# Kernel tuning notes

Measured on AMD Instinct MI355X. Metric: run time of the kernel, lower is better.

The kernel has to match this reference:

```python
import jax, jax.numpy as jnp
import numpy as np

HIDDEN = 1024
N_HEADS = 16
HEAD_DIM = HIDDEN // N_HEADS
LN_EPS = 1e-5


def setup_inputs() -> dict:
    key = jax.random.key(0)
    ks = jax.random.split(key, 8)
    B, S = 4, 1024
    inp = {
        'input_tensor': jax.random.normal(ks[0], (B, S, HIDDEN), dtype=jnp.float32),
        'memory_tensor': jax.random.normal(ks[1], (B, S, HIDDEN), dtype=jnp.float32),
        'attention_mask': jnp.ones((B, S, S), dtype=jnp.float32),
        'wq': jax.random.normal(ks[2], (HIDDEN, HIDDEN), dtype=jnp.float32) * 0.02,
        'wk': jax.random.normal(ks[3], (HIDDEN, HIDDEN), dtype=jnp.float32) * 0.02,
        'wv': jax.random.normal(ks[4], (HIDDEN, HIDDEN), dtype=jnp.float32) * 0.02,
        'wo': jax.random.normal(ks[5], (HIDDEN, HIDDEN), dtype=jnp.float32) * 0.02,
        'ln_gamma': jnp.ones((HIDDEN,), dtype=jnp.float32),
        'ln_beta': jnp.zeros((HIDDEN,), dtype=jnp.float32),
        'seq_length': 1024,
        'enc_seq_length': 1024,
    }
    return inp


def _layernorm(x, gamma, beta):
    mu = jnp.mean(x, axis=-1, keepdims=True)
    var = jnp.mean(jnp.square(x - mu), axis=-1, keepdims=True)
    return (x - mu) * jax.lax.rsqrt(var + LN_EPS) * gamma + beta


def reference(input_tensor, memory_tensor, attention_mask, wq, wk, wv, wo,
              ln_gamma, ln_beta, seq_length, enc_seq_length):
    B = input_tensor.shape[0]
    S = seq_length
    x2d = input_tensor.reshape(-1, HIDDEN)            # [B*S, H]
    normed = _layernorm(x2d, ln_gamma, ln_beta)       # LayerPreprocess
    # is_encdec_att=False: memory = normed output (memory_tensor unused)
    mem = normed
    # torch nn.Linear(bias=False): y = x @ W.T
    q = (normed @ wq.T).reshape(B, S, N_HEADS, HEAD_DIM).transpose(0, 2, 1, 3)
    k = (mem @ wk.T).reshape(B, S, N_HEADS, HEAD_DIM).transpose(0, 2, 1, 3)
    v = (mem @ wv.T).reshape(B, S, N_HEADS, HEAD_DIM).transpose(0, 2, 1, 3)
    scale = 1.0 / np.sqrt(float(HEAD_DIM))
    scores = jnp.einsum('bhqd,bhkd->bhqk', q, k) * scale   # [B, H, S, S]
    scores = scores - 10000.0 * (1.0 - attention_mask[:, None, :, :])
    probs = jax.nn.softmax(scores, axis=-1)
    ctx = jnp.einsum('bhqk,bhkd->bhqd', probs, v)          # [B, H, S, dh]
    ctx = ctx.transpose(0, 2, 1, 3).reshape(B * S, HIDDEN)
    attn_out = ctx @ wo.T
    # LayerPostprocess (dropout=0): residual add with raw (pre-LN) input
    return attn_out + x2d
```

## Files before the change

### kernel.cpp

```cpp
#include <hip/hip_runtime.h>
#include <hip/hip_bf16.h>


typedef unsigned short u16;
typedef __attribute__((ext_vector_type(8))) short short8;
typedef __attribute__((ext_vector_type(4))) float f32x4;

__device__ __forceinline__ u16 f2bf(float f) {
  union { float f; unsigned u; } cv; cv.f = f;
  unsigned u = cv.u + 0x7fffu + ((cv.u >> 16) & 1u);
  return (u16)(u >> 16);
}

__device__ __forceinline__ float bf2f(u16 u) {
  union { unsigned u; float f; } cv; cv.u = ((unsigned)u) << 16;
  return cv.f;
}

__device__ __forceinline__ void gload_lds16(const void* g, void* l) {
  __builtin_amdgcn_global_load_lds(
      (const __attribute__((address_space(1))) void*)g,
      (__attribute__((address_space(3))) void*)l, 16, 0, 0);
}

__device__ __forceinline__ f32x4 mfma16(short8 a, short8 b, f32x4 c) {
  return __builtin_amdgcn_mfma_f32_16x16x32_bf16(a, b, c, 0, 0, 0);
}

__global__ __launch_bounds__(256) void ln_kernel(const float* __restrict__ x,
                                                 const float* __restrict__ gamma,
                                                 const float* __restrict__ beta,
                                                 u16* __restrict__ outn) {
  __shared__ float sm[4];
  const int row = blockIdx.x, t = threadIdx.x;
  float4 v = ((const float4*)(x + (size_t)row * 1024))[t];
  float s = v.x + v.y + v.z + v.w;
#pragma unroll
  for (int off = 32; off; off >>= 1) s += __shfl_down(s, off);
  if ((t & 63) == 0) sm[t >> 6] = s;
  __syncthreads();
  const float mu = (sm[0] + sm[1] + sm[2] + sm[3]) * (1.0f / 1024.0f);
  const float dx = v.x - mu, dy = v.y - mu, dz = v.z - mu, dw = v.w - mu;
  float vs = dx * dx + dy * dy + dz * dz + dw * dw;
  __syncthreads();
#pragma unroll
  for (int off = 32; off; off >>= 1) vs += __shfl_down(vs, off);
  if ((t & 63) == 0) sm[t >> 6] = vs;
  __syncthreads();
  const float var = (sm[0] + sm[1] + sm[2] + sm[3]) * (1.0f / 1024.0f);
  const float rstd = rsqrtf(var + 1e-5f);
  float4 g = ((const float4*)gamma)[t];
  float4 b = ((const float4*)beta)[t];
  uint2 pk;
  pk.x = (unsigned)f2bf(dx * rstd * g.x + b.x) | ((unsigned)f2bf(dy * rstd * g.y + b.y) << 16);
  pk.y = (unsigned)f2bf(dz * rstd * g.z + b.z) | ((unsigned)f2bf(dw * rstd * g.w + b.w) << 16);
  *(uint2*)&outn[(size_t)row * 1024 + t * 4] = pk;
}

__global__ __launch_bounds__(256) void cvt_w(const float* __restrict__ wq,
                                             const float* __restrict__ wk,
                                             const float* __restrict__ wv,
                                             const float* __restrict__ wo,
                                             u16* __restrict__ out) {
  const int i = blockIdx.x * 256 + threadIdx.x;
  const int e = i * 4;
  const int seg = e >> 20;
  const int off = e & 1048575;
  const float* src = (seg == 0) ? wq : (seg == 1) ? wk : (seg == 2) ? wv : wo;
  float4 v = *(const float4*)(src + off);
  uint2 pk;
  pk.x = (unsigned)f2bf(v.x) | ((unsigned)f2bf(v.y) << 16);
  pk.y = (unsigned)f2bf(v.z) | ((unsigned)f2bf(v.w) << 16);
  *(uint2*)&out[e] = pk;
}

__global__ __launch_bounds__(256) void cvt_bias(const float* __restrict__ mask,
                                                u16* __restrict__ bias) {
  const int tid = blockIdx.x * 256 + threadIdx.x;
  const int half = tid & 1;
  const int lg = (tid >> 1) & 3;
  const int kt = (tid >> 3) & 15;
  const int q  = (tid >> 7) & 1023;
  const int b  = tid >> 17;
  const float* src = mask + ((size_t)b * 1024 + q) * 1024 + kt * 64 + lg * 4;
  float4 v0 = *(const float4*)(src + (half * 2 + 0) * 16);
  float4 v1 = *(const float4*)(src + (half * 2 + 1) * 16);
  uint4 w;
  w.x = (unsigned)f2bf(fmaf(10000.f, v0.x, -10000.f)) |
        ((unsigned)f2bf(fmaf(10000.f, v0.y, -10000.f)) << 16);
  w.y = (unsigned)f2bf(fmaf(10000.f, v0.z, -10000.f)) |
        ((unsigned)f2bf(fmaf(10000.f, v0.w, -10000.f)) << 16);
  w.z = (unsigned)f2bf(fmaf(10000.f, v1.x, -10000.f)) |
        ((unsigned)f2bf(fmaf(10000.f, v1.y, -10000.f)) << 16);
  w.w = (unsigned)f2bf(fmaf(10000.f, v1.z, -10000.f)) |
        ((unsigned)f2bf(fmaf(10000.f, v1.w, -10000.f)) << 16);
  *(uint4*)&bias[(size_t)tid * 8] = w;
}

template <int MODE>
__global__ __launch_bounds__(256) void gemm_bt(const u16* __restrict__ A,
                                               const u16* __restrict__ Bm,
                                               u16* __restrict__ outQ, u16* __restrict__ outK,
                                               u16* __restrict__ outVt,
                                               float* __restrict__ outF,
                                               const float* __restrict__ resid) {
  constexpr int BK = 64, KK = 1024;
  __shared__ u16 As[128 * BK];
  __shared__ u16 Bs[128 * BK];
  const int m0 = blockIdx.y * 128, n0 = blockIdx.x * 128;
  const int t = threadIdx.x;
  const int wid = t >> 6, lane = t & 63;
  const int wm = (wid >> 1) * 64, wn = (wid & 1) * 64;
  const int lr = lane & 15, lg = lane >> 4;
  f32x4 acc[4][4] = {};
  const u16* aSrc = A + (size_t)(m0 + (t >> 3)) * KK + (t & 7) * 8;
  const u16* bSrc = Bm + (size_t)(n0 + (t >> 3)) * KK + (t & 7) * 8;

  for (int k0 = 0; k0 < KK; k0 += BK) {
    __syncthreads();
#pragma unroll
    for (int c = 0; c < 4; c++) {
      gload_lds16(aSrc + (size_t)c * 32 * KK + k0, As + c * 2048 + t * 8);
      gload_lds16(bSrc + (size_t)c * 32 * KK + k0, Bs + c * 2048 + t * 8);
    }
    __syncthreads();
    short8 af[4][2], bfr[4][2];
#pragma unroll
    for (int mi = 0; mi < 4; mi++)
#pragma unroll
      for (int kc = 0; kc < 2; kc++)
        af[mi][kc] = *(const short8*)&As[(wm + mi * 16 + lr) * BK + kc * 32 + lg * 8];
#pragma unroll
    for (int ni = 0; ni < 4; ni++)
#pragma unroll
      for (int kc = 0; kc < 2; kc++)
        bfr[ni][kc] = *(const short8*)&Bs[(wn + ni * 16 + lr) * BK + kc * 32 + lg * 8];
#pragma unroll
    for (int mi = 0; mi < 4; mi++)
#pragma unroll
      for (int ni = 0; ni < 4; ni++)
#pragma unroll
        for (int kc = 0; kc < 2; kc++)
          acc[mi][ni] = mfma16(af[mi][kc], bfr[ni][kc], acc[mi][ni]);
  }

#pragma unroll
  for (int mi = 0; mi < 4; mi++)
#pragma unroll
    for (int ni = 0; ni < 4; ni++)
#pragma unroll
      for (int r = 0; r < 4; r++) {
        const int i = m0 + wm + mi * 16 + lg * 4 + r;
        const int j = n0 + wn + ni * 16 + lr;
        const float val = acc[mi][ni][r];
        if (MODE == 0) {
          const int seg = j >> 10, jj = j & 1023;
          const int h = jj >> 6, d = jj & 63;
          const int b = i >> 10, s_ = i & 1023;
          if (seg == 0)      outQ[((size_t)(b * 16 + h) * 1024 + s_) * 64 + d] = f2bf(val * 0.125f);
          else if (seg == 1) outK[((size_t)(b * 16 + h) * 1024 + s_) * 64 + d] = f2bf(val);
          else               outVt[((size_t)(b * 16 + h) * 64 + d) * 1024 + s_] = f2bf(val);
        } else {
          const size_t o = (size_t)i * 1024 + j;
          outF[o] = val + resid[o];
        }
      }
}

__global__ __launch_bounds__(256) void flash_kernel(const u16* __restrict__ Qg,
                                                    const u16* __restrict__ Kg,
                                                    const u16* __restrict__ Vt,
                                                    const u16* __restrict__ bias,
                                                    u16* __restrict__ ctx) {
  const int h = blockIdx.x, qt = blockIdx.y, b = blockIdx.z;
  const int bh = b * 16 + h;
  __shared__ u16 Ks[2][4096];
  __shared__ u16 Vs[2][4096];
  __shared__ u16 Ps[4][1024];
  const int t = threadIdx.x, wid = t >> 6, lane = t & 63;
  const int lr = lane & 15, lg = lane >> 4;
  const int hR = lr & 7;
  const int qbase = qt * 64 + wid * 16;

  short8 qf0, qf1;
  {
    const u16* qrow = Qg + ((size_t)bh * 1024 + qbase + lr) * 64;
    qf0 = *(const short8*)(qrow + lg * 8);
    qf1 = *(const short8*)(qrow + 32 + lg * 8);
  }
  f32x4 octx[4] = {};
  float m_ln = -1e30f, l_ln = 0.0f;

  const u16* kS0 = Kg + (size_t)bh * 65536;
  const u16* vS0 = Vt + (size_t)bh * 65536;
  const int srow = t >> 3, scb = t & 7;

  const u16* bptr = bias + ((size_t)b * 1024 + qbase + lr) * 1024 + lg * 16;

  auto STAGE = [&](int nb, int kt) {
#pragma unroll
    for (int c = 0; c < 2; c++) {
      const int row = c * 32 + srow;
      const int sc = (scb ^ (row & 7)) * 8;
      gload_lds16(kS0 + (size_t)(kt * 64 + row) * 64 + sc, &Ks[nb][c * 2048 + t * 8]);
      gload_lds16(vS0 + (size_t)row * 1024 + kt * 64 + sc, &Vs[nb][c * 2048 + t * 8]);
    }
  };

  STAGE(0, 0);
  short8 bc0 = *(const short8*)(bptr);
  short8 bc1 = *(const short8*)(bptr + 8);
  asm volatile("s_waitcnt vmcnt(0)" ::: "memory");
  __builtin_amdgcn_s_barrier();
  __builtin_amdgcn_sched_barrier(0);

  int cur = 0;
  for (int kt = 0; kt < 16; kt++) {
    const int ktn = (kt < 15) ? kt + 1 : 15;
    STAGE(cur ^ 1, ktn);
    short8 bn0 = *(const short8*)(bptr + ktn * 64);
    short8 bn1 = *(const short8*)(bptr + ktn * 64 + 8);

    float sv[4][4];
#pragma unroll
    for (int kn = 0; kn < 4; kn++) {
      const int R = kn * 16 + lr;
      short8 kf0 = *(const short8*)&Ks[cur][R * 64 + ((lg ^ hR) << 3)];
      short8 kf1 = *(const short8*)&Ks[cur][R * 64 + (((lg + 4) ^ hR) << 3)];
      f32x4 s = {};
      s = mfma16(kf0, qf0, s);
      s = mfma16(kf1, qf1, s);
      short8 bsel = (kn < 2) ? bc0 : bc1;
#pragma unroll
      for (int r = 0; r < 4; r++)
        sv[kn][r] = s[r] + bf2f((u16)bsel[(kn & 1) * 4 + r]);
    }

    float mx0 = fmaxf(fmaxf(sv[0][0], sv[0][1]), fmaxf(sv[0][2], sv[0][3]));
    float mx1 = fmaxf(fmaxf(sv[1][0], sv[1][1]), fmaxf(sv[1][2], sv[1][3]));
    float mx2 = fmaxf(fmaxf(sv[2][0], sv[2][1]), fmaxf(sv[2][2], sv[2][3]));
    float mx3 = fmaxf(fmaxf(sv[3][0], sv[3][1]), fmaxf(sv[3][2], sv[3][3]));
    float mt = fmaxf(fmaxf(mx0, mx1), fmaxf(mx2, mx3));
    mt = fmaxf(mt, __shfl_xor(mt, 16));
    mt = fmaxf(mt, __shfl_xor(mt, 32));
    const float mn = fmaxf(m_ln, mt);
    const float f = __expf(m_ln - mn);
    m_ln = mn;
    float ps = 0.0f;
#pragma unroll
    for (int kn = 0; kn < 4; kn++) {
      float p0 = __expf(sv[kn][0] - mn), p1 = __expf(sv[kn][1] - mn);
      float p2 = __expf(sv[kn][2] - mn), p3 = __expf(sv[kn][3] - mn);
      sv[kn][0] = p0; sv[kn][1] = p1; sv[kn][2] = p2; sv[kn][3] = p3;
      ps += (p0 + p1) + (p2 + p3);
    }
    ps += __shfl_xor(ps, 16);
    ps += __shfl_xor(ps, 32);
    l_ln = l_ln * f + ps;

    float fb[4];
#pragma unroll
    for (int r = 0; r < 4; r++)
      fb[r] = __shfl(f, (lane & 48) | (lg * 4 + r), 64);
#pragma unroll
    for (int g = 0; g < 4; g++)
#pragma unroll
      for (int r = 0; r < 4; r++) octx[g][r] *= fb[r];

    const int swz = (lr & 7) << 1;
#pragma unroll
    for (int kn = 0; kn < 4; kn++) {
      uint2 w;
      w.x = (unsigned)f2bf(sv[kn][0]) | ((unsigned)f2bf(sv[kn][1]) << 16);
      w.y = (unsigned)f2bf(sv[kn][2]) | ((unsigned)f2bf(sv[kn][3]) << 16);
      *(uint2*)&Ps[wid][lr * 64 + (((kn * 4 + lg) ^ swz) << 2)] = w;
    }
    short8 pa0 = *(const short8*)&Ps[wid][lr * 64 + (((2 * lg) ^ swz) << 2)];
    short8 pa1 = *(const short8*)&Ps[wid][lr * 64 + (((8 + 2 * lg) ^ swz) << 2)];

#pragma unroll
    for (int g = 0; g < 4; g++) {
      const int R = g * 16 + lr;
      short8 vf0 = *(const short8*)&Vs[cur][R * 64 + ((lg ^ hR) << 3)];
      short8 vf1 = *(const short8*)&Vs[cur][R * 64 + (((lg + 4) ^ hR) << 3)];
      octx[g] = mfma16(pa0, vf0, octx[g]);
      octx[g] = mfma16(pa1, vf1, octx[g]);
    }

    asm volatile("s_waitcnt vmcnt(0)" ::: "memory");
    __builtin_amdgcn_s_barrier();
    __builtin_amdgcn_sched_barrier(0);
    cur ^= 1;
    bc0 = bn0; bc1 = bn1;
  }

  float lb[4];
#pragma unroll
  for (int r = 0; r < 4; r++)
    lb[r] = __shfl(l_ln, (lane & 48) | (lg * 4 + r), 64);
#pragma unroll
  for (int g = 0; g < 4; g++)
#pragma unroll
    for (int r = 0; r < 4; r++) {
      const int qr = qbase + lg * 4 + r;
      ctx[((size_t)b * 1024 + qr) * 1024 + h * 64 + g * 16 + lr] = f2bf(octx[g][r] / lb[r]);
    }
}

extern "C" void kernel_launch(void* const* d_in, const int* in_sizes, int n_in,
                              void* d_out, int out_size, void* d_ws, size_t ws_size,
                              hipStream_t stream) {
  const float* x     = (const float*)d_in[0];
  const float* mask  = (const float*)d_in[2];
  const float* wq    = (const float*)d_in[3];
  const float* wk    = (const float*)d_in[4];
  const float* wv    = (const float*)d_in[5];
  const float* wo    = (const float*)d_in[6];
  const float* gamma = (const float*)d_in[7];
  const float* beta  = (const float*)d_in[8];
  float* out = (float*)d_out;

  char* ws = (char*)d_ws;
  u16* normed = (u16*)(ws);
  u16* wcat   = (u16*)(ws + (8ull << 20));
  u16* Qg     = (u16*)(ws + (16ull << 20));
  u16* Kg     = (u16*)(ws + (24ull << 20));
  u16* Vtg    = (u16*)(ws + (32ull << 20));
  u16* ctx    = (u16*)(ws + (40ull << 20));
  u16* wo_bf  = wcat + 3072ull * 1024;
  u16* bias   = normed;

  ln_kernel<<<4096, 256, 0, stream>>>(x, gamma, beta, normed);
  cvt_w<<<4096, 256, 0, stream>>>(wq, wk, wv, wo, wcat);
  gemm_bt<0><<<dim3(24, 32), 256, 0, stream>>>(normed, wcat, Qg, Kg, Vtg, nullptr, nullptr);
  cvt_bias<<<2048, 256, 0, stream>>>(mask, bias);
  flash_kernel<<<dim3(16, 16, 4), 256, 0, stream>>>(Qg, Kg, Vtg, bias, ctx);
  gemm_bt<1><<<dim3(8, 32), 256, 0, stream>>>(ctx, wo_bf, nullptr, nullptr, nullptr, out, x);
}
```

Measured before the change: 254.4 us.

## Double-buffer GEMM, stage epilogue through LDS, read fp32 mask directly in flash

The GEMM now uses BK=32 double-buffered LDS staging with a swizzled layout, and s_setprio around the MFMA block. The QKV epilogue goes through LDS so Q/K/Vt are written with vectorised, coalesced stores instead of scattered 2-byte stores. The output GEMM uses 64-row tiles so it launches more blocks. The cvt_bias pass is removed and the flash kernel reads the fp32 mask directly, computing the additive bias in registers, at the cost of twice the mask bytes per tile and more registers.

```diff
diff --git a/kernel.cpp b/kernel.cpp
--- a/kernel.cpp
+++ b/kernel.cpp
@@ -10,11 +10,6 @@
   union { float f; unsigned u; } cv; cv.f = f;
   unsigned u = cv.u + 0x7fffu + ((cv.u >> 16) & 1u);
   return (u16)(u >> 16);
-}
-
-__device__ __forceinline__ float bf2f(u16 u) {
-  union { unsigned u; float f; } cv; cv.u = ((unsigned)u) << 16;
-  return cv.f;
 }
 
 __device__ __forceinline__ void gload_lds16(const void* g, void* l) {
@@ -74,29 +69,6 @@
   *(uint2*)&out[e] = pk;
 }
 
-__global__ __launch_bounds__(256) void cvt_bias(const float* __restrict__ mask,
-                                                u16* __restrict__ bias) {
-  const int tid = blockIdx.x * 256 + threadIdx.x;
-  const int half = tid & 1;
-  const int lg = (tid >> 1) & 3;
-  const int kt = (tid >> 3) & 15;
-  const int q  = (tid >> 7) & 1023;
-  const int b  = tid >> 17;
-  const float* src = mask + ((size_t)b * 1024 + q) * 1024 + kt * 64 + lg * 4;
-  float4 v0 = *(const float4*)(src + (half * 2 + 0) * 16);
-  float4 v1 = *(const float4*)(src + (half * 2 + 1) * 16);
-  uint4 w;
-  w.x = (unsigned)f2bf(fmaf(10000.f, v0.x, -10000.f)) |
-        ((unsigned)f2bf(fmaf(10000.f, v0.y, -10000.f)) << 16);
-  w.y = (unsigned)f2bf(fmaf(10000.f, v0.z, -10000.f)) |
-        ((unsigned)f2bf(fmaf(10000.f, v0.w, -10000.f)) << 16);
-  w.z = (unsigned)f2bf(fmaf(10000.f, v1.x, -10000.f)) |
-        ((unsigned)f2bf(fmaf(10000.f, v1.y, -10000.f)) << 16);
-  w.w = (unsigned)f2bf(fmaf(10000.f, v1.z, -10000.f)) |
-        ((unsigned)f2bf(fmaf(10000.f, v1.w, -10000.f)) << 16);
-  *(uint4*)&bias[(size_t)tid * 8] = w;
-}
-
 template <int MODE>
 __global__ __launch_bounds__(256) void gemm_bt(const u16* __restrict__ A,
                                                const u16* __restrict__ Bm,
@@ -104,73 +76,135 @@
                                                u16* __restrict__ outVt,
                                                float* __restrict__ outF,
                                                const float* __restrict__ resid) {
-  constexpr int BK = 64, KK = 1024;
-  __shared__ u16 As[128 * BK];
-  __shared__ u16 Bs[128 * BK];
-  const int m0 = blockIdx.y * 128, n0 = blockIdx.x * 128;
+  constexpr int BM = (MODE == 0) ? 128 : 64;
+  constexpr int MI = BM / 32;
+  constexpr int ASZ = BM * 32;
+  constexpr int BSZ = 128 * 32;
+  constexpr int STG = 2 * ASZ + 2 * BSZ;
+  constexpr int SMEM = (MODE == 0) ? (STG > 18432 ? STG : 18432) : STG;
+  __shared__ u16 sm[SMEM];
+
+  const int m0 = blockIdx.y * BM, n0 = blockIdx.x * 128;
   const int t = threadIdx.x;
   const int wid = t >> 6, lane = t & 63;
-  const int wm = (wid >> 1) * 64, wn = (wid & 1) * 64;
+  const int wm = (wid >> 1) * (BM / 2), wn = (wid & 1) * 64;
   const int lr = lane & 15, lg = lane >> 4;
-  f32x4 acc[4][4] = {};
-  const u16* aSrc = A + (size_t)(m0 + (t >> 3)) * KK + (t & 7) * 8;
-  const u16* bSrc = Bm + (size_t)(n0 + (t >> 3)) * KK + (t & 7) * 8;
-
-  for (int k0 = 0; k0 < KK; k0 += BK) {
+  const int swz = (lg ^ ((lr >> 1) & 3)) << 3;
+  f32x4 acc[MI][4] = {};
+
+  const int scol = (((t & 3) ^ ((t >> 3) & 3)) << 3);
+  const u16* aT = A + (size_t)(m0 + (t >> 2)) * 1024 + scol;
+  const u16* bT = Bm + (size_t)(n0 + (t >> 2)) * 1024 + scol;
+
+  auto STAGE = [&](int buf, int kt) {
+    const int k0 = kt * 32;
+#pragma unroll
+    for (int cc = 0; cc < BM / 64; cc++)
+      gload_lds16(aT + (size_t)cc * 65536 + k0, &sm[buf * ASZ + cc * 2048 + t * 8]);
+#pragma unroll
+    for (int cc = 0; cc < 2; cc++)
+      gload_lds16(bT + (size_t)cc * 65536 + k0, &sm[2 * ASZ + buf * BSZ + cc * 2048 + t * 8]);
+  };
+
+  STAGE(0, 0);
+  asm volatile("s_waitcnt vmcnt(0)" ::: "memory");
+  __builtin_amdgcn_s_barrier();
+  __builtin_amdgcn_sched_barrier(0);
+
+  int cur = 0;
+  for (int kt = 0; kt < 32; kt++) {
+    STAGE(cur ^ 1, (kt + 1) & 31);
+
+    short8 af[MI], bfr[4];
+#pragma unroll
+    for (int mi = 0; mi < MI; mi++)
+      af[mi] = *(const short8*)&sm[cur * ASZ + (wm + mi * 16 + lr) * 32 + swz];
+#pragma unroll
+    for (int ni = 0; ni < 4; ni++)
+      bfr[ni] = *(const short8*)&sm[2 * ASZ + cur * BSZ + (wn + ni * 16 + lr) * 32 + swz];
+    __builtin_amdgcn_s_setprio(1);
+#pragma unroll
+    for (int mi = 0; mi < MI; mi++)
+#pragma unroll
+      for (int ni = 0; ni < 4; ni++)
+        acc[mi][ni] = mfma16(af[mi], bfr[ni], acc[mi][ni]);
+    __builtin_amdgcn_s_setprio(0);
+
+    asm volatile("s_waitcnt vmcnt(0)" ::: "memory");
+    __builtin_amdgcn_s_barrier();
+    __builtin_amdgcn_sched_barrier(0);
+    cur ^= 1;
+  }
+
+  if (MODE == 1) {
+#pragma unroll
+    for (int mi = 0; mi < MI; mi++)
+#pragma unroll
+      for (int ni = 0; ni < 4; ni++)
+#pragma unroll
+        for (int r = 0; r < 4; r++) {
+          const int i = m0 + wm + mi * 16 + lg * 4 + r;
+          const int j = n0 + wn + ni * 16 + lr;
+          const size_t o = (size_t)i * 1024 + j;
+          outF[o] = acc[mi][ni][r] + resid[o];
+        }
+    return;
+  }
+
+  const int seg = (n0 + wn) >> 10;
+  const int g8 = lane >> 3, j8 = lane & 7;
+  if (seg < 2) {
+    u16* epi = &sm[wid * 4608];
+    const float qs = (seg == 0) ? 0.125f : 1.0f;
+#pragma unroll
+    for (int mi = 0; mi < 4; mi++)
+#pragma unroll
+      for (int ni = 0; ni < 4; ni++)
+#pragma unroll
+        for (int r = 0; r < 4; r++)
+          epi[(mi * 16 + lg * 4 + r) * 72 + ni * 16 + lr] = f2bf(acc[mi][ni][r] * qs);
     __syncthreads();
-#pragma unroll
-    for (int c = 0; c < 4; c++) {
-      gload_lds16(aSrc + (size_t)c * 32 * KK + k0, As + c * 2048 + t * 8);
-      gload_lds16(bSrc + (size_t)c * 32 * KK + k0, Bs + c * 2048 + t * 8);
-    }
+    u16* dst = (seg == 0) ? outQ : outK;
+    const int h = ((n0 + wn) & 1023) >> 6;
+#pragma unroll
+    for (int it = 0; it < 8; it++) {
+      const int ml = it * 8 + g8;
+      short8 v = *(const short8*)&epi[ml * 72 + j8 * 8];
+      const int i = m0 + wm + ml;
+      const int b = i >> 10, s_ = i & 1023;
+      *(short8*)&dst[((size_t)(b * 16 + h) * 1024 + s_) * 64 + j8 * 8] = v;
+    }
+  } else {
+    u16* epi = &sm[wid * 4096];
+#pragma unroll
+    for (int mi = 0; mi < 4; mi++)
+#pragma unroll
+      for (int ni = 0; ni < 4; ni++) {
+        const int n = ni * 16 + lr;
+        const int c2 = 4 * mi + lg;
+        uint2 w;
+        w.x = (unsigned)f2bf(acc[mi][ni][0]) | ((unsigned)f2bf(acc[mi][ni][1]) << 16);
+        w.y = (unsigned)f2bf(acc[mi][ni][2]) | ((unsigned)f2bf(acc[mi][ni][3]) << 16);
+        *(uint2*)&epi[n * 64 + ((c2 ^ (n & 15)) << 2)] = w;
+      }
     __syncthreads();
-    short8 af[4][2], bfr[4][2];
-#pragma unroll
-    for (int mi = 0; mi < 4; mi++)
-#pragma unroll
-      for (int kc = 0; kc < 2; kc++)
-        af[mi][kc] = *(const short8*)&As[(wm + mi * 16 + lr) * BK + kc * 32 + lg * 8];
-#pragma unroll
-    for (int ni = 0; ni < 4; ni++)
-#pragma unroll
-      for (int kc = 0; kc < 2; kc++)
-        bfr[ni][kc] = *(const short8*)&Bs[(wn + ni * 16 + lr) * BK + kc * 32 + lg * 8];
-#pragma unroll
-    for (int mi = 0; mi < 4; mi++)
-#pragma unroll
-      for (int ni = 0; ni < 4; ni++)
-#pragma unroll
-        for (int kc = 0; kc < 2; kc++)
-          acc[mi][ni] = mfma16(af[mi][kc], bfr[ni][kc], acc[mi][ni]);
-  }
-
-#pragma unroll
-  for (int mi = 0; mi < 4; mi++)
-#pragma unroll
-    for (int ni = 0; ni < 4; ni++)
-#pragma unroll
-      for (int r = 0; r < 4; r++) {
-        const int i = m0 + wm + mi * 16 + lg * 4 + r;
-        const int j = n0 + wn + ni * 16 + lr;
-        const float val = acc[mi][ni][r];
-        if (MODE == 0) {
-          const int seg = j >> 10, jj = j & 1023;
-          const int h = jj >> 6, d = jj & 63;
-          const int b = i >> 10, s_ = i & 1023;
-          if (seg == 0)      outQ[((size_t)(b * 16 + h) * 1024 + s_) * 64 + d] = f2bf(val * 0.125f);
-          else if (seg == 1) outK[((size_t)(b * 16 + h) * 1024 + s_) * 64 + d] = f2bf(val);
-          else               outVt[((size_t)(b * 16 + h) * 64 + d) * 1024 + s_] = f2bf(val);
-        } else {
-          const size_t o = (size_t)i * 1024 + j;
-          outF[o] = val + resid[o];
-        }
-      }
+    const int h = ((n0 + wn) & 1023) >> 6;
+    const int b = (m0 + wm) >> 10, sb = (m0 + wm) & 1023;
+#pragma unroll
+    for (int it = 0; it < 8; it++) {
+      const int n = it * 8 + g8;
+      uint2 w0 = *(const uint2*)&epi[n * 64 + (((2 * j8) ^ (n & 15)) << 2)];
+      uint2 w1 = *(const uint2*)&epi[n * 64 + (((2 * j8 + 1) ^ (n & 15)) << 2)];
+      uint4 w; w.x = w0.x; w.y = w0.y; w.z = w1.x; w.w = w1.y;
+      *(uint4*)&outVt[((size_t)(b * 16 + h) * 64 + n) * 1024 + sb + j8 * 8] = w;
+    }
+  }
 }
 
 __global__ __launch_bounds__(256) void flash_kernel(const u16* __restrict__ Qg,
                                                     const u16* __restrict__ Kg,
                                                     const u16* __restrict__ Vt,
-                                                    const u16* __restrict__ bias,
+                                                    const float* __restrict__ mask,
                                                     u16* __restrict__ ctx) {
   const int h = blockIdx.x, qt = blockIdx.y, b = blockIdx.z;
   const int bh = b * 16 + h;
@@ -195,7 +229,7 @@
   const u16* vS0 = Vt + (size_t)bh * 65536;
   const int srow = t >> 3, scb = t & 7;
 
-  const u16* bptr = bias + ((size_t)b * 1024 + qbase + lr) * 1024 + lg * 16;
+  const float* mptr = mask + ((size_t)b * 1024 + qbase + lr) * 1024 + lg * 4;
 
   auto STAGE = [&](int nb, int kt) {
 #pragma unroll
@@ -208,8 +242,12 @@
   };
 
   STAGE(0, 0);
-  short8 bc0 = *(const short8*)(bptr);
-  short8 bc1 = *(const short8*)(bptr + 8);
+  float mc[4][4];
+#pragma unroll
+  for (int kn = 0; kn < 4; kn++) {
+    float4 v = *(const float4*)(mptr + kn * 16);
+    mc[kn][0] = v.x; mc[kn][1] = v.y; mc[kn][2] = v.z; mc[kn][3] = v.w;
+  }
   asm volatile("s_waitcnt vmcnt(0)" ::: "memory");
   __builtin_amdgcn_s_barrier();
   __builtin_amdgcn_sched_barrier(0);
@@ -218,8 +256,12 @@
   for (int kt = 0; kt < 16; kt++) {
     const int ktn = (kt < 15) ? kt + 1 : 15;
     STAGE(cur ^ 1, ktn);
-    short8 bn0 = *(const short8*)(bptr + ktn * 64);
-    short8 bn1 = *(const short8*)(bptr + ktn * 64 + 8);
+    float mnx[4][4];
+#pragma unroll
+    for (int kn = 0; kn < 4; kn++) {
+      float4 v = *(const float4*)(mptr + ktn * 64 + kn * 16);
+      mnx[kn][0] = v.x; mnx[kn][1] = v.y; mnx[kn][2] = v.z; mnx[kn][3] = v.w;
+    }
 
     float sv[4][4];
 #pragma unroll
@@ -230,10 +272,10 @@
       f32x4 s = {};
       s = mfma16(kf0, qf0, s);
       s = mfma16(kf1, qf1, s);
-      short8 bsel = (kn < 2) ? bc0 : bc1;
+      __builtin_amdgcn_s_setprio(0);
 #pragma unroll
       for (int r = 0; r < 4; r++)
-        sv[kn][r] = s[r] + bf2f((u16)bsel[(kn & 1) * 4 + r]);
+        sv[kn][r] = s[r] + fmaf(10000.f, mc[kn][r], -10000.f);
     }
 
     float mx0 = fmaxf(fmaxf(sv[0][0], sv[0][1]), fmaxf(sv[0][2], sv[0][3]));
@@ -267,17 +309,18 @@
 #pragma unroll
       for (int r = 0; r < 4; r++) octx[g][r] *= fb[r];
 
-    const int swz = (lr & 7) << 1;
+    const int pswz = (lr & 7) << 1;
 #pragma unroll
     for (int kn = 0; kn < 4; kn++) {
       uint2 w;
       w.x = (unsigned)f2bf(sv[kn][0]) | ((unsigned)f2bf(sv[kn][1]) << 16);
       w.y = (unsigned)f2bf(sv[kn][2]) | ((unsigned)f2bf(sv[kn][3]) << 16);
-      *(uint2*)&Ps[wid][lr * 64 + (((kn * 4 + lg) ^ swz) << 2)] = w;
-    }
-    short8 pa0 = *(const short8*)&Ps[wid][lr * 64 + (((2 * lg) ^ swz) << 2)];
-    short8 pa1 = *(const short8*)&Ps[wid][lr * 64 + (((8 + 2 * lg) ^ swz) << 2)];
-
+      *(uint2*)&Ps[wid][lr * 64 + (((kn * 4 + lg) ^ pswz) << 2)] = w;
+    }
+    short8 pa0 = *(const short8*)&Ps[wid][lr * 64 + (((2 * lg) ^ pswz) << 2)];
+    short8 pa1 = *(const short8*)&Ps[wid][lr * 64 + (((8 + 2 * lg) ^ pswz) << 2)];
+
+    __builtin_amdgcn_s_setprio(1);
 #pragma unroll
     for (int g = 0; g < 4; g++) {
       const int R = g * 16 + lr;
@@ -286,12 +329,16 @@
       octx[g] = mfma16(pa0, vf0, octx[g]);
       octx[g] = mfma16(pa1, vf1, octx[g]);
     }
+    __builtin_amdgcn_s_setprio(0);
 
     asm volatile("s_waitcnt vmcnt(0)" ::: "memory");
     __builtin_amdgcn_s_barrier();
     __builtin_amdgcn_sched_barrier(0);
     cur ^= 1;
-    bc0 = bn0; bc1 = bn1;
+#pragma unroll
+    for (int kn = 0; kn < 4; kn++)
+#pragma unroll
+      for (int r = 0; r < 4; r++) mc[kn][r] = mnx[kn][r];
   }
 
   float lb[4];
@@ -328,12 +375,10 @@
   u16* Vtg    = (u16*)(ws + (32ull << 20));
   u16* ctx    = (u16*)(ws + (40ull << 20));
   u16* wo_bf  = wcat + 3072ull * 1024;
-  u16* bias   = normed;
 
   ln_kernel<<<4096, 256, 0, stream>>>(x, gamma, beta, normed);
   cvt_w<<<4096, 256, 0, stream>>>(wq, wk, wv, wo, wcat);
   gemm_bt<0><<<dim3(24, 32), 256, 0, stream>>>(normed, wcat, Qg, Kg, Vtg, nullptr, nullptr);
-  cvt_bias<<<2048, 256, 0, stream>>>(mask, bias);
-  flash_kernel<<<dim3(16, 16, 4), 256, 0, stream>>>(Qg, Kg, Vtg, bias, ctx);
-  gemm_bt<1><<<dim3(8, 32), 256, 0, stream>>>(ctx, wo_bf, nullptr, nullptr, nullptr, out, x);
-}
+  flash_kernel<<<dim3(16, 16, 4), 256, 0, stream>>>(Qg, Kg, Vtg, mask, ctx);
+  gemm_bt<1><<<dim3(8, 64), 256, 0, stream>>>(ctx, wo_bf, nullptr, nullptr, nullptr, out, x);
+}
```

Measured after the change: 223.3 us. -12.2%, faster.
